# Optimization experiments

Hardware: AMD Instinct MI355X
Metric: run time of the kernel (lower is better)

The kernel has to match this reference:

```python
import jax, jax.numpy as jnp
import numpy as np

N, IN_DIM, HID, HEADS, HOPS, NCLS, E = 20000, 1536, 256, 4, 3, 3, 320000
HD = HID // HEADS
EPS = 1e-5
NEG_SLOPE = 0.2


def layer_norm(x, g, b):
    mu = jnp.mean(x, axis=-1, keepdims=True)
    var = jnp.var(x, axis=-1, keepdims=True)
    return (x - mu) * jax.lax.rsqrt(var + EPS) * g + b


def gatv2(x, src, dst, Wl, bl, Wr, br, att, bias):
    # x: [N, HID]; src/dst: [E'] (self loops included)
    xl = (x @ Wl + bl).reshape(N, HEADS, HD)  # source transform
    xr = (x @ Wr + br).reshape(N, HEADS, HD)  # target transform
    e = jax.nn.leaky_relu(xl[src] + xr[dst], NEG_SLOPE)          # [E', H, D]
    logits = jnp.einsum('ehd,hd->eh', e, att)                     # [E', H]
    m = jax.ops.segment_max(logits, dst, num_segments=N)         # [N, H]
    ex = jnp.exp(logits - m[dst])
    denom = jax.ops.segment_sum(ex, dst, num_segments=N)
    alpha = ex / denom[dst]                                       # softmax per dst
    msg = xl[src] * alpha[:, :, None]                             # [E', H, D]
    out = jax.ops.segment_sum(msg, dst, num_segments=N)
    return out.reshape(N, HID) + bias


def setup_inputs() -> dict:
    key = jax.random.key(0)
    ks = jax.random.split(key, 20)
    s = lambda k, shp, sc: jax.random.normal(k, shp, jnp.float32) * sc
    return {
        'features': s(ks[0], (N, IN_DIM), 1.0),
        'edge_index': jax.random.randint(ks[1], (2, E), 0, N, jnp.int64),
        'proj_W': s(ks[2], (IN_DIM, HID), 0.02),
        'proj_b': jnp.zeros((HID,), jnp.float32),
        'n0_g': jnp.ones((HID,), jnp.float32),
        'n0_b': jnp.zeros((HID,), jnp.float32),
        'Wl': s(ks[3], (HOPS, HID, HID), 0.05),
        'bl': jnp.zeros((HOPS, HID), jnp.float32),
        'Wr': s(ks[4], (HOPS, HID, HID), 0.05),
        'br': jnp.zeros((HOPS, HID), jnp.float32),
        'att': s(ks[5], (HOPS, HEADS, HD), 0.1),
        'gbias': jnp.zeros((HOPS, HID), jnp.float32),
        'ln_g': jnp.ones((HOPS, HID), jnp.float32),
        'ln_b': jnp.zeros((HOPS, HID), jnp.float32),
        'h1_W': s(ks[6], (HID, HID), 0.05),
        'h1_b': jnp.zeros((HID,), jnp.float32),
        'h2_W': s(ks[7], (HID, NCLS), 0.05),
        'h2_b': jnp.zeros((NCLS,), jnp.float32),
    }


def reference(features, edge_index, proj_W, proj_b, n0_g, n0_b, Wl, bl, Wr, br,
              att, gbias, ln_g, ln_b, h1_W, h1_b, h2_W, h2_b):
    # add self loops (PyG GATv2Conv default)
    loop = jnp.arange(N, dtype=edge_index.dtype)
    src = jnp.concatenate([edge_index[0], loop])
    dst = jnp.concatenate([edge_index[1], loop])

    x = layer_norm(features @ proj_W + proj_b, n0_g, n0_b)
    for h in range(HOPS):
        g = gatv2(x, src, dst, Wl[h], bl[h], Wr[h], br[h], att[h], gbias[h])
        x = layer_norm(g + x, ln_g[h], ln_b[h])
    # head (dropout inactive at eval); torch GELU is exact erf form
    x = jax.nn.gelu(x @ h1_W + h1_b, approximate=False)
    return x @ h2_W + h2_b
```

## Files before the change

kernel.cpp:

```cpp
#include <hip/hip_runtime.h>
#include <hip/hip_bf16.h>
#include <math.h>

#define NN 20000
#define INDIM 1536
#define HID 256
#define NE 320000
#define NEDGE (NE + NN)
#define EPSV 1e-5f
#define NEG 0.2f

typedef unsigned short ushort_b;
typedef unsigned int uint32;
typedef __bf16 bf16x8 __attribute__((ext_vector_type(8)));
typedef float f32x4 __attribute__((ext_vector_type(4)));

#define AS1(p) ((const __attribute__((address_space(1))) void*)(p))
#define AS3(p) ((__attribute__((address_space(3))) void*)(p))

__device__ inline ushort_b f2bf(float x) {
  union { float f; uint32 u; } v; v.f = x;
  uint32 r = v.u + 0x7FFFu + ((v.u >> 16) & 1u);
  return (ushort_b)(r >> 16);
}
__device__ inline float bf2f(ushort_b h) {
  union { uint32 u; float f; } v; v.u = ((uint32)h) << 16;
  return v.f;
}
__device__ inline float u2f(uint32 u) {
  union { uint32 u; float f; } v; v.u = u; return v.f;
}
__device__ inline uint32 cvtpk_bf16(float a, float b) {
  uint32 r;
  asm("v_cvt_pk_bf16_f32 %0, %1, %2" : "=v"(r) : "v"(a), "v"(b));
  return r;
}
__device__ inline float4 ldbf4(const ushort_b* p) {
  ushort4 u = *(const ushort4*)p;
  float4 f;
  f.x = bf2f(u.x); f.y = bf2f(u.y); f.z = bf2f(u.z); f.w = bf2f(u.w);
  return f;
}
__device__ inline float4 us4f(ushort4 u) {
  float4 f;
  f.x = bf2f(u.x); f.y = bf2f(u.y); f.z = bf2f(u.z); f.w = bf2f(u.w);
  return f;
}

template<int OUTMODE, int DUALB>
__global__ __launch_bounds__(256, 3) void gemm_mfma(
    const float* __restrict__ Af,
    const ushort_b* __restrict__ Bt0, const ushort_b* __restrict__ Bt1,
    const float* __restrict__ bias0, const float* __restrict__ bias1,
    void* __restrict__ C0, void* __restrict__ C1,
    int Mstore, int Kloop, int Kstride)
{
  __shared__ ushort_b Bs[3 * 8192];
  const ushort_b* Bt;
  const float* bias;
  void* Cv;
  int kbase;
  if (DUALB) {
    Bt = blockIdx.z ? Bt1 : Bt0;
    bias = blockIdx.z ? bias1 : bias0;
    Cv = blockIdx.z ? C1 : C0;
    kbase = 0;
  } else {
    Bt = Bt0;
    bias = blockIdx.z ? bias1 : bias0;
    Cv = (float*)C0 + (size_t)blockIdx.z * NN * HID;
    kbase = blockIdx.z * Kloop;
  }

  int tid = threadIdx.x;
  int wave = tid >> 6, lane = tid & 63;
  int quad = lane >> 4, mrow = lane & 15;
  int r0 = blockIdx.y * 128;
  int p  = blockIdx.x;
  int nk = Kloop >> 5;
  int nchunk = Kstride >> 5;
  int cb = kbase >> 5;

  int arow0 = r0 + (wave << 5) + mrow;
  int arow1 = arow0 + 16;
  if (arow0 >= Mstore) arow0 = Mstore - 1;
  if (arow1 >= Mstore) arow1 = Mstore - 1;
  const float* Aptr0 = Af + (size_t)arow0 * Kstride + kbase + (quad << 3);
  const float* Aptr1 = Af + (size_t)arow1 * Kstride + kbase + (quad << 3);

  f32x4 acc[2][8] = {};
  float pA0[16], pA1[16];

  auto issueB = [&](int kc, int buf) {
    const char* g = (const char*)Bt + (((size_t)(p * nchunk + (cb + kc))) << 14);
    char* l = (char*)Bs + buf * 16384;
    int o = tid << 4;
#pragma unroll
    for (int pl = 0; pl < 2; pl++) {
      int off = (pl << 13) + o;
      __builtin_amdgcn_global_load_lds(AS1(g + off), AS3(l + off), 16, 0, 0);
      __builtin_amdgcn_global_load_lds(AS1(g + off + 4096), AS3(l + off + 4096), 16, 0, 0);
    }
  };
  auto loadA = [&](int k, float* dst) {
    const float* s0 = Aptr0 + (k << 5);
    const float* s1 = Aptr1 + (k << 5);
    *(float4*)(dst)      = *(const float4*)(s0);
    *(float4*)(dst + 4)  = *(const float4*)(s0 + 4);
    *(float4*)(dst + 8)  = *(const float4*)(s1);
    *(float4*)(dst + 12) = *(const float4*)(s1 + 4);
  };
  auto cvtFrag = [&](const float* s, bf16x8& hh, bf16x8& ll) {
    union { bf16x8 v; uint32 u[4]; } H, L;
#pragma unroll
    for (int q2 = 0; q2 < 4; q2++) {
      float a = s[2 * q2], b = s[2 * q2 + 1];
      uint32 hp = cvtpk_bf16(a, b);
      float fa = u2f(hp << 16);
      float fb = u2f(hp & 0xffff0000u);
      H.u[q2] = hp;
      L.u[q2] = cvtpk_bf16(a - fa, b - fb);
    }
    hh = H.v; ll = L.v;
  };
  auto computeStage = [&](int buf, const bf16x8& ah0, const bf16x8& al0,
                          const bf16x8& ah1, const bf16x8& al1) {
    const ushort_b* bp = Bs + buf * 8192;
#pragma unroll
    for (int u = 0; u < 8; u++) {
      bf16x8 bh = *(const bf16x8*)(bp + (u << 9) + (lane << 3));
      bf16x8 bl = *(const bf16x8*)(bp + 4096 + (u << 9) + (lane << 3));
      acc[0][u] = __builtin_amdgcn_mfma_f32_16x16x32_bf16(ah0, bh, acc[0][u], 0, 0, 0);
      acc[0][u] = __builtin_amdgcn_mfma_f32_16x16x32_bf16(al0, bh, acc[0][u], 0, 0, 0);
      acc[0][u] = __builtin_amdgcn_mfma_f32_16x16x32_bf16(ah0, bl, acc[0][u], 0, 0, 0);
      acc[1][u] = __builtin_amdgcn_mfma_f32_16x16x32_bf16(ah1, bh, acc[1][u], 0, 0, 0);
      acc[1][u] = __builtin_amdgcn_mfma_f32_16x16x32_bf16(al1, bh, acc[1][u], 0, 0, 0);
      acc[1][u] = __builtin_amdgcn_mfma_f32_16x16x32_bf16(ah1, bl, acc[1][u], 0, 0, 0);
    }
  };

  loadA(0, pA0);
  issueB(0, 0);
  issueB(1, 1);
  loadA(1, pA1);
  asm volatile("s_waitcnt vmcnt(8)" ::: "memory");
  __builtin_amdgcn_sched_barrier(0);
  __builtin_amdgcn_s_barrier();
  __builtin_amdgcn_sched_barrier(0);

  int bcur = 0;
  for (int k = 0; k < nk; k += 2) {
    int b1 = bcur + 1; if (b1 >= 3) b1 -= 3;
    int b2 = bcur + 2; if (b2 >= 3) b2 -= 3;

    {
      bf16x8 ah0, al0, ah1, al1;
      cvtFrag(pA0, ah0, al0);
      cvtFrag(pA0 + 8, ah1, al1);
      if (k + 2 < nk) { issueB(k + 2, b2); loadA(k + 2, pA0); }
      computeStage(bcur, ah0, al0, ah1, al1);
      if (k + 2 < nk) { asm volatile("s_waitcnt vmcnt(8)" ::: "memory"); }
      else            { asm volatile("s_waitcnt vmcnt(4)" ::: "memory"); }
      __builtin_amdgcn_sched_barrier(0);
      __builtin_amdgcn_s_barrier();
      __builtin_amdgcn_sched_barrier(0);
    }
    {
      bf16x8 ah0, al0, ah1, al1;
      cvtFrag(pA1, ah0, al0);
      cvtFrag(pA1 + 8, ah1, al1);
      if (k + 3 < nk) { issueB(k + 3, bcur); loadA(k + 3, pA1); }
      computeStage(b1, ah0, al0, ah1, al1);
      if (k + 3 < nk) {
        asm volatile("s_waitcnt vmcnt(8)" ::: "memory");
        __builtin_amdgcn_sched_barrier(0);
        __builtin_amdgcn_s_barrier();
        __builtin_amdgcn_sched_barrier(0);
      }
    }
    bcur = b2;
  }

#pragma unroll
  for (int u = 0; u < 8; u++) {
    int col = (p << 7) + (u << 4) + mrow;
    float bb = bias[col];
#pragma unroll
    for (int t = 0; t < 2; t++) {
#pragma unroll
      for (int r = 0; r < 4; r++) {
        int row = r0 + (wave << 5) + (t << 4) + (quad << 2) + r;
        if (row < Mstore) {
          float v = acc[t][u][r] + bb;
          if (OUTMODE == 3) v = 0.5f * v * (1.f + erff(v * 0.70710678118654752f));
          if (OUTMODE == 2) ((ushort_b*)Cv)[(size_t)row * 256 + col] = f2bf(v);
          else              ((float*)Cv)[(size_t)row * 256 + col] = v;
        }
      }
    }
  }
}

__device__ inline void prep_body(const float* __restrict__ W, int ldw, int nchunk,
                                 ushort_b* __restrict__ out, int c, int p, int tid)
{
  ushort_b* base = out + (((size_t)(p * nchunk + c)) << 13);
#pragma unroll
  for (int g0 = 0; g0 < 2; g0++) {
    int g = tid + (g0 << 8);
    int u = g >> 6, l = g & 63;
    int quad = l >> 4, mrow = l & 15;
    int col = (p << 7) + (u << 4) + mrow;
    int krow = (c << 5) + (quad << 3);
    uint32 hu[4], lu[4];
#pragma unroll
    for (int q2 = 0; q2 < 4; q2++) {
      float a = W[(size_t)(krow + 2 * q2) * ldw + col];
      float b = W[(size_t)(krow + 2 * q2 + 1) * ldw + col];
      ushort_b h0 = f2bf(a), h1 = f2bf(b);
      hu[q2] = (uint32)h0 | ((uint32)h1 << 16);
      lu[q2] = (uint32)f2bf(a - bf2f(h0)) | ((uint32)f2bf(b - bf2f(h1)) << 16);
    }
    *(uint4*)(base + (size_t)g * 8)        = make_uint4(hu[0], hu[1], hu[2], hu[3]);
    *(uint4*)(base + 4096 + (size_t)g * 8) = make_uint4(lu[0], lu[1], lu[2], lu[3]);
  }
}

__global__ __launch_bounds__(256) void prep_frag(
    const float* __restrict__ W, int ldw, int nchunk, ushort_b* __restrict__ out)
{
  prep_body(W, ldw, nchunk, out, blockIdx.x, blockIdx.y, threadIdx.x);
}

__global__ __launch_bounds__(256) void prep_frag7(
    const float* __restrict__ Wl, const float* __restrict__ Wr,
    const float* __restrict__ h1W, ushort_b* __restrict__ dst)
{
  int z = blockIdx.z;
  const float* W = (z < 3) ? Wl + (size_t)z * 65536
                 : (z < 6) ? Wr + (size_t)(z - 3) * 65536
                           : h1W;
  prep_body(W, 256, 8, dst + (size_t)z * 131072, blockIdx.x, blockIdx.y, threadIdx.x);
}

__global__ __launch_bounds__(256) void ln_sum_kernel(
    const float* __restrict__ in,
    const float* __restrict__ g, const float* __restrict__ b,
    float* __restrict__ out, int n)
{
  int wave = threadIdx.x >> 6, lane = threadIdx.x & 63;
  int row = blockIdx.x * 4 + wave;
  if (row >= n) return;
  int c = lane << 2;
  const float* p0 = in + (size_t)row * HID + c;
  float4 v  = *(const float4*)(p0);
  float4 v1 = *(const float4*)(p0 + (size_t)NN * HID);
  float4 v2 = *(const float4*)(p0 + (size_t)2 * NN * HID);
  float4 v3 = *(const float4*)(p0 + (size_t)3 * NN * HID);
  v.x += v1.x + v2.x + v3.x;
  v.y += v1.y + v2.y + v3.y;
  v.z += v1.z + v2.z + v3.z;
  v.w += v1.w + v2.w + v3.w;
  float s1 = v.x + v.y + v.z + v.w;
  float s2 = v.x * v.x + v.y * v.y + v.z * v.z + v.w * v.w;
#pragma unroll
  for (int m = 1; m < 64; m <<= 1) {
    s1 += __shfl_xor(s1, m, 64);
    s2 += __shfl_xor(s2, m, 64);
  }
  float mu = s1 * (1.f / 256.f);
  float var = s2 * (1.f / 256.f) - mu * mu;
  float rstd = rsqrtf(var + EPSV);
  float4 gv = *(const float4*)(g + c);
  float4 bv = *(const float4*)(b + c);
  float4 o;
  o.x = (v.x - mu) * rstd * gv.x + bv.x;
  o.y = (v.y - mu) * rstd * gv.y + bv.y;
  o.z = (v.z - mu) * rstd * gv.z + bv.z;
  o.w = (v.w - mu) * rstd * gv.w + bv.w;
  *(float4*)(out + (size_t)row * HID + c) = o;
}

__global__ void count_kernel(const int* __restrict__ ei, int* __restrict__ cnt)
{
  int e = blockIdx.x * blockDim.x + threadIdx.x;
  if (e < NEDGE) {
    int d = (e < NE) ? ei[NE + e] : (e - NE);
    atomicAdd(&cnt[d], 1);
  }
}

__global__ __launch_bounds__(1024) void scan_kernel(
    const int* __restrict__ cnt, int* __restrict__ offs, int* __restrict__ cursor)
{
  __shared__ int sums[1024];
  int tid = threadIdx.x;
  const int CH = 20;
  int base = tid * CH;
  int loc[CH];
  int s = 0;
#pragma unroll
  for (int i = 0; i < CH; i++) {
    int idx = base + i;
    int v = (idx < NN) ? cnt[idx] : 0;
    loc[i] = s;
    s += v;
  }
  sums[tid] = s;
  __syncthreads();
  for (int off = 1; off < 1024; off <<= 1) {
    int t = (tid >= off) ? sums[tid - off] : 0;
    __syncthreads();
    sums[tid] += t;
    __syncthreads();
  }
  int pre = (tid == 0) ? 0 : sums[tid - 1];
#pragma unroll
  for (int i = 0; i < CH; i++) {
    int idx = base + i;
    if (idx < NN) { int e = pre + loc[i]; offs[idx] = e; cursor[idx] = e; }
  }
  if (tid == 0) offs[NN] = NEDGE;
}

__global__ void scatter_kernel(const int* __restrict__ ei, int* __restrict__ cursor,
                               int* __restrict__ csr_src)
{
  int e = blockIdx.x * blockDim.x + threadIdx.x;
  if (e < NEDGE) {
    int s, d;
    if (e < NE) { s = ei[e]; d = ei[NE + e]; }
    else { s = e - NE; d = e - NE; }
    int p = atomicAdd(&cursor[d], 1);
    csr_src[p] = s;
  }
}

__device__ inline float edge_logit(float4 xv, float4 xrv, float4 attv) {
  float e0 = xv.x + xrv.x, e1 = xv.y + xrv.y, e2 = xv.z + xrv.z, e3 = xv.w + xrv.w;
  e0 = (e0 > 0.f) ? e0 : NEG * e0;
  e1 = (e1 > 0.f) ? e1 : NEG * e1;
  e2 = (e2 > 0.f) ? e2 : NEG * e2;
  e3 = (e3 > 0.f) ? e3 : NEG * e3;
  float lc = e0 * attv.x + e1 * attv.y + e2 * attv.z + e3 * attv.w;
  lc += __shfl_xor(lc, 1, 16);
  lc += __shfl_xor(lc, 2, 16);
  lc += __shfl_xor(lc, 4, 16);
  lc += __shfl_xor(lc, 8, 16);
  return lc;
}

#define ACCUM(i, wt, xv) {                             \
    lS[i] += wt;                                       \
    pS##i##0 += wt * xv.x; pS##i##1 += wt * xv.y;      \
    pS##i##2 += wt * xv.z; pS##i##3 += wt * xv.w; }

__global__ __launch_bounds__(256) void gat_kernel(
    const ushort_b* __restrict__ xl, const ushort_b* __restrict__ xr,
    const float* __restrict__ x_in, const float* __restrict__ att,
    const float* __restrict__ gbias, const float* __restrict__ ln_g,
    const float* __restrict__ ln_b, const int* __restrict__ offs,
    const int* __restrict__ csr_src, float* __restrict__ x_out)
{
  int wave = threadIdx.x >> 6, lane = threadIdx.x & 63;
  int node = blockIdx.x * 4 + wave;
  int c = lane << 2;
  float4 xrv = ldbf4(xr + (size_t)node * HID + c);
  float4 attv = *(const float4*)(att + c);

  float lS[4] = {0.f, 0.f, 0.f, 0.f};
  float pS00 = 0.f, pS01 = 0.f, pS02 = 0.f, pS03 = 0.f;
  float pS10 = 0.f, pS11 = 0.f, pS12 = 0.f, pS13 = 0.f;
  float pS20 = 0.f, pS21 = 0.f, pS22 = 0.f, pS23 = 0.f;
  float pS30 = 0.f, pS31 = 0.f, pS32 = 0.f, pS33 = 0.f;

  int e = offs[node], end = offs[node + 1];
  int last = end - 1;

  int s1i = e + 1 <= last ? e + 1 : last;
  int s2i = e + 2 <= last ? e + 2 : last;
  int s3i = e + 3 <= last ? e + 3 : last;
  int i0 = csr_src[e], i1 = csr_src[s1i], i2 = csr_src[s2i], i3 = csr_src[s3i];
  ushort4 a0 = *(const ushort4*)(xl + (size_t)i0 * HID + c);
  ushort4 a1 = *(const ushort4*)(xl + (size_t)i1 * HID + c);
  ushort4 a2 = *(const ushort4*)(xl + (size_t)i2 * HID + c);
  ushort4 a3 = *(const ushort4*)(xl + (size_t)i3 * HID + c);

  for (;;) {
    int rem = end - e;
    int en = e + 4;
    bool more = en < end;
    ushort4 b0, b1, b2, b3;
    if (more) {
      int t1i = en + 1 <= last ? en + 1 : last;
      int t2i = en + 2 <= last ? en + 2 : last;
      int t3i = en + 3 <= last ? en + 3 : last;
      int j0 = csr_src[en], j1 = csr_src[t1i], j2 = csr_src[t2i], j3 = csr_src[t3i];
      b0 = *(const ushort4*)(xl + (size_t)j0 * HID + c);
      b1 = *(const ushort4*)(xl + (size_t)j1 * HID + c);
      b2 = *(const ushort4*)(xl + (size_t)j2 * HID + c);
      b3 = *(const ushort4*)(xl + (size_t)j3 * HID + c);
    }
    float4 x0v = us4f(a0);
    float4 x1v = us4f(a1);
    float4 x2v = us4f(a2);
    float4 x3v = us4f(a3);
    float g0 = edge_logit(x0v, xrv, attv);
    float g1 = edge_logit(x1v, xrv, attv);
    float g2 = edge_logit(x2v, xrv, attv);
    float g3 = edge_logit(x3v, xrv, attv);
    float w0 = __expf(g0);
    float w1 = (rem > 1) ? __expf(g1) : 0.f;
    float w2 = (rem > 2) ? __expf(g2) : 0.f;
    float w3 = (rem > 3) ? __expf(g3) : 0.f;
    ACCUM(0, w0, x0v);
    ACCUM(1, w1, x1v);
    ACCUM(2, w2, x2v);
    ACCUM(3, w3, x3v);
    if (!more) break;
    e = en;
    a0 = b0; a1 = b1; a2 = b2; a3 = b3;
  }

  float l  = lS[0] + lS[1] + lS[2] + lS[3];
  float q0 = pS00 + pS10 + pS20 + pS30;
  float q1 = pS01 + pS11 + pS21 + pS31;
  float q2 = pS02 + pS12 + pS22 + pS32;
  float q3 = pS03 + pS13 + pS23 + pS33;

  float inv = 1.f / l;
  float4 xv = *(const float4*)(x_in + (size_t)node * HID + c);
  float4 gb = *(const float4*)(gbias + c);
  float o0 = q0 * inv + gb.x + xv.x;
  float o1 = q1 * inv + gb.y + xv.y;
  float o2 = q2 * inv + gb.z + xv.z;
  float o3 = q3 * inv + gb.w + xv.w;
  float s1s = o0 + o1 + o2 + o3;
  float s2s = o0 * o0 + o1 * o1 + o2 * o2 + o3 * o3;
#pragma unroll
  for (int mmk = 1; mmk < 64; mmk <<= 1) {
    s1s += __shfl_xor(s1s, mmk, 64);
    s2s += __shfl_xor(s2s, mmk, 64);
  }
  float mu = s1s * (1.f / 256.f);
  float var = s2s * (1.f / 256.f) - mu * mu;
  float rstd = rsqrtf(var + EPSV);
  float4 gv = *(const float4*)(ln_g + c);
  float4 bv = *(const float4*)(ln_b + c);
  float4 o;
  o.x = (o0 - mu) * rstd * gv.x + bv.x;
  o.y = (o1 - mu) * rstd * gv.y + bv.y;
  o.z = (o2 - mu) * rstd * gv.z + bv.z;
  o.w = (o3 - mu) * rstd * gv.w + bv.w;
  *(float4*)(x_out + (size_t)node * HID + c) = o;
}

__global__ __launch_bounds__(256) void head2_kernel(
    const float* __restrict__ t1, const float* __restrict__ W,
    const float* __restrict__ bias, float* __restrict__ out)
{
  int wave = threadIdx.x >> 6, lane = threadIdx.x & 63;
  int row = blockIdx.x * 4 + wave;
  if (row >= NN) return;
  int c = lane << 2;
  float4 v = *(const float4*)(t1 + (size_t)row * HID + c);
  float p0 = 0.f, p1 = 0.f, p2 = 0.f;
#pragma unroll
  for (int j = 0; j < 4; j++) {
    float vj = (&v.x)[j];
    p0 += vj * W[(c + j) * 3 + 0];
    p1 += vj * W[(c + j) * 3 + 1];
    p2 += vj * W[(c + j) * 3 + 2];
  }
#pragma unroll
  for (int mm = 1; mm < 64; mm <<= 1) {
    p0 += __shfl_xor(p0, mm, 64);
    p1 += __shfl_xor(p1, mm, 64);
    p2 += __shfl_xor(p2, mm, 64);
  }
  if (lane == 0) {
    out[(size_t)row * 3 + 0] = p0 + bias[0];
    out[(size_t)row * 3 + 1] = p1 + bias[1];
    out[(size_t)row * 3 + 2] = p2 + bias[2];
  }
}

extern "C" void kernel_launch(void* const* d_in, const int* in_sizes, int n_in,
                              void* d_out, int out_size, void* d_ws, size_t ws_size,
                              hipStream_t stream)
{
  const float* features = (const float*)d_in[0];
  const int*   ei       = (const int*)d_in[1];
  const float* proj_W   = (const float*)d_in[2];
  const float* proj_b   = (const float*)d_in[3];
  const float* n0_g     = (const float*)d_in[4];
  const float* n0_b     = (const float*)d_in[5];
  const float* Wl       = (const float*)d_in[6];
  const float* bl       = (const float*)d_in[7];
  const float* Wr       = (const float*)d_in[8];
  const float* br       = (const float*)d_in[9];
  const float* att      = (const float*)d_in[10];
  const float* gbias    = (const float*)d_in[11];
  const float* ln_g     = (const float*)d_in[12];
  const float* ln_b     = (const float*)d_in[13];
  const float* h1_W     = (const float*)d_in[14];
  const float* h1_b     = (const float*)d_in[15];
  const float* h2_W     = (const float*)d_in[16];
  const float* h2_b     = (const float*)d_in[17];
  float* out = (float*)d_out;

  char* w = (char*)d_ws;
  float*    x0    = (float*)w;    w += (size_t)NN * HID * 4;
  float*    x1    = (float*)w;    w += (size_t)NN * HID * 4;
  float*    part1 = (float*)w;    w += (size_t)NN * HID * 4;
  ushort_b* xlb   = (ushort_b*)w; w += (size_t)NN * HID * 2;
  ushort_b* xrb   = (ushort_b*)w; w += (size_t)NN * HID * 2;
  ushort_b* wtp   = (ushort_b*)w; w += (size_t)2 * HID * INDIM * 2;
  ushort_b* w7    = (ushort_b*)w; w += (size_t)14 * HID * HID * 2;
  float* zbias = (float*)w; w += (size_t)HID * 4;
  int* cnt     = (int*)w;  w += (size_t)NN * 4;
  int* offs    = (int*)w;  w += (size_t)(NN + 1) * 4;
  int* cursor  = (int*)w;  w += (size_t)NN * 4;
  int* csr     = (int*)w;  w += (size_t)NEDGE * 4;

  hipMemsetAsync(cnt, 0, (size_t)NN * 4, stream);
  hipMemsetAsync(zbias, 0, (size_t)HID * 4, stream);
  count_kernel<<<(NEDGE + 255) / 256, 256, 0, stream>>>(ei, cnt);
  scan_kernel<<<1, 1024, 0, stream>>>(cnt, offs, cursor);
  scatter_kernel<<<(NEDGE + 255) / 256, 256, 0, stream>>>(ei, cursor, csr);

  prep_frag<<<dim3(INDIM / 32, 2), 256, 0, stream>>>(proj_W, HID, INDIM / 32, wtp);
  prep_frag7<<<dim3(8, 2, 7), 256, 0, stream>>>(Wl, Wr, h1_W, w7);

  const int MB = (NN + 127) / 128;
  dim3 gproj(2, MB, 4);
  dim3 ghop(2, MB, 2);
  dim3 gsingle(2, MB, 1);

  gemm_mfma<0, 0><<<gproj, 256, 0, stream>>>(
      features, wtp, wtp, proj_b, zbias, x0, x0, NN, INDIM / 4, INDIM);
  ln_sum_kernel<<<(NN + 3) / 4, 256, 0, stream>>>(x0, n0_g, n0_b, x0, NN);

  float* xcur = x0;
  float* xnxt = x1;
  for (int h = 0; h < 3; h++) {
    gemm_mfma<2, 1><<<ghop, 256, 0, stream>>>(
        xcur, w7 + (size_t)h * 131072, w7 + (size_t)(3 + h) * 131072,
        bl + h * HID, br + h * HID, xlb, xrb, NN, HID, HID);
    gat_kernel<<<NN / 4, 256, 0, stream>>>(
        xlb, xrb, xcur, att + h * HID, gbias + h * HID,
        ln_g + h * HID, ln_b + h * HID, offs, csr, xnxt);
    float* t = xcur; xcur = xnxt; xnxt = t;
  }

  gemm_mfma<3, 1><<<gsingle, 256, 0, stream>>>(
      xcur, w7 + (size_t)6 * 131072, w7 + (size_t)6 * 131072,
      h1_b, h1_b, part1, part1, NN, HID, HID);
  head2_kernel<<<(NN + 3) / 4, 256, 0, stream>>>(part1, h2_W, h2_b, out);
}
```

Baseline: 603.7 us.

## Merge prep kernels, halve projection split-K, deepen GAT index prefetch

Merges the two weight-fragment prep kernels into one launch and folds the zbias memset into count_kernel, which cuts launch count. Changes the projection GEMM split-K from 4 to 2 slices, so the LN reduction kernel reads two partials instead of four. The GAT kernel now loads CSR source indices two batches ahead and adds a launch-bounds occupancy hint. Fewer K-slices means fewer GEMM blocks and less parallelism, but less partial-sum traffic.

```diff
diff --git a/kernel.cpp b/kernel.cpp
--- a/kernel.cpp
+++ b/kernel.cpp
@@ -226,21 +226,21 @@
   }
 }
 
-__global__ __launch_bounds__(256) void prep_frag(
-    const float* __restrict__ W, int ldw, int nchunk, ushort_b* __restrict__ out)
-{
-  prep_body(W, ldw, nchunk, out, blockIdx.x, blockIdx.y, threadIdx.x);
-}
-
-__global__ __launch_bounds__(256) void prep_frag7(
-    const float* __restrict__ Wl, const float* __restrict__ Wr,
-    const float* __restrict__ h1W, ushort_b* __restrict__ dst)
-{
-  int z = blockIdx.z;
-  const float* W = (z < 3) ? Wl + (size_t)z * 65536
-                 : (z < 6) ? Wr + (size_t)(z - 3) * 65536
-                           : h1W;
-  prep_body(W, 256, 8, dst + (size_t)z * 131072, blockIdx.x, blockIdx.y, threadIdx.x);
+__global__ __launch_bounds__(256) void prep_all(
+    const float* __restrict__ projW, const float* __restrict__ Wl,
+    const float* __restrict__ Wr, const float* __restrict__ h1W,
+    ushort_b* __restrict__ wtp, ushort_b* __restrict__ w7)
+{
+  int z = blockIdx.z, c = blockIdx.x, p = blockIdx.y;
+  if (z == 7) {
+    prep_body(projW, HID, INDIM / 32, wtp, c, p, threadIdx.x);
+  } else {
+    if (c >= 8) return;
+    const float* W = (z < 3) ? Wl + (size_t)z * 65536
+                   : (z < 6) ? Wr + (size_t)(z - 3) * 65536
+                             : h1W;
+    prep_body(W, 256, 8, w7 + (size_t)z * 131072, c, p, threadIdx.x);
+  }
 }
 
 __global__ __launch_bounds__(256) void ln_sum_kernel(
@@ -255,12 +255,7 @@
   const float* p0 = in + (size_t)row * HID + c;
   float4 v  = *(const float4*)(p0);
   float4 v1 = *(const float4*)(p0 + (size_t)NN * HID);
-  float4 v2 = *(const float4*)(p0 + (size_t)2 * NN * HID);
-  float4 v3 = *(const float4*)(p0 + (size_t)3 * NN * HID);
-  v.x += v1.x + v2.x + v3.x;
-  v.y += v1.y + v2.y + v3.y;
-  v.z += v1.z + v2.z + v3.z;
-  v.w += v1.w + v2.w + v3.w;
+  v.x += v1.x; v.y += v1.y; v.z += v1.z; v.w += v1.w;
   float s1 = v.x + v.y + v.z + v.w;
   float s2 = v.x * v.x + v.y * v.y + v.z * v.z + v.w * v.w;
 #pragma unroll
@@ -281,9 +276,11 @@
   *(float4*)(out + (size_t)row * HID + c) = o;
 }
 
-__global__ void count_kernel(const int* __restrict__ ei, int* __restrict__ cnt)
+__global__ void count_kernel(const int* __restrict__ ei, int* __restrict__ cnt,
+                             float* __restrict__ zbias)
 {
   int e = blockIdx.x * blockDim.x + threadIdx.x;
+  if (e < HID) zbias[e] = 0.f;
   if (e < NEDGE) {
     int d = (e < NE) ? ei[NE + e] : (e - NE);
     atomicAdd(&cnt[d], 1);
@@ -355,7 +352,7 @@
     pS##i##0 += wt * xv.x; pS##i##1 += wt * xv.y;      \
     pS##i##2 += wt * xv.z; pS##i##3 += wt * xv.w; }
 
-__global__ __launch_bounds__(256) void gat_kernel(
+__global__ __launch_bounds__(256, 6) void gat_kernel(
     const ushort_b* __restrict__ xl, const ushort_b* __restrict__ xr,
     const float* __restrict__ x_in, const float* __restrict__ att,
     const float* __restrict__ gbias, const float* __restrict__ ln_g,
@@ -376,30 +373,31 @@
 
   int e = offs[node], end = offs[node + 1];
   int last = end - 1;
-
-  int s1i = e + 1 <= last ? e + 1 : last;
-  int s2i = e + 2 <= last ? e + 2 : last;
-  int s3i = e + 3 <= last ? e + 3 : last;
-  int i0 = csr_src[e], i1 = csr_src[s1i], i2 = csr_src[s2i], i3 = csr_src[s3i];
-  ushort4 a0 = *(const ushort4*)(xl + (size_t)i0 * HID + c);
-  ushort4 a1 = *(const ushort4*)(xl + (size_t)i1 * HID + c);
-  ushort4 a2 = *(const ushort4*)(xl + (size_t)i2 * HID + c);
-  ushort4 a3 = *(const ushort4*)(xl + (size_t)i3 * HID + c);
+#define CI(x) ((x) <= last ? (x) : last)
+  auto G = [&](int i) { return *(const ushort4*)(xl + (size_t)i * HID + c); };
+
+  int i0 = csr_src[e], i1 = csr_src[CI(e + 1)];
+  int i2 = csr_src[CI(e + 2)], i3 = csr_src[CI(e + 3)];
+  ushort4 a0 = G(i0), a1 = G(i1), a2 = G(i2), a3 = G(i3);
+  int en = e + 4;
+  bool more = en < end;
+  int j0, j1, j2, j3;
+  if (more) {
+    j0 = csr_src[en]; j1 = csr_src[CI(en + 1)];
+    j2 = csr_src[CI(en + 2)]; j3 = csr_src[CI(en + 3)];
+  }
 
   for (;;) {
     int rem = end - e;
-    int en = e + 4;
-    bool more = en < end;
+    int en2 = en + 4;
+    bool more2 = more && (en2 < end);
     ushort4 b0, b1, b2, b3;
     if (more) {
-      int t1i = en + 1 <= last ? en + 1 : last;
-      int t2i = en + 2 <= last ? en + 2 : last;
-      int t3i = en + 3 <= last ? en + 3 : last;
-      int j0 = csr_src[en], j1 = csr_src[t1i], j2 = csr_src[t2i], j3 = csr_src[t3i];
-      b0 = *(const ushort4*)(xl + (size_t)j0 * HID + c);
-      b1 = *(const ushort4*)(xl + (size_t)j1 * HID + c);
-      b2 = *(const ushort4*)(xl + (size_t)j2 * HID + c);
-      b3 = *(const ushort4*)(xl + (size_t)j3 * HID + c);
+      b0 = G(j0); b1 = G(j1); b2 = G(j2); b3 = G(j3);
+      if (more2) {
+        j0 = csr_src[en2]; j1 = csr_src[CI(en2 + 1)];
+        j2 = csr_src[CI(en2 + 2)]; j3 = csr_src[CI(en2 + 3)];
+      }
     }
     float4 x0v = us4f(a0);
     float4 x1v = us4f(a1);
@@ -418,9 +416,10 @@
     ACCUM(2, w2, x2v);
     ACCUM(3, w3, x3v);
     if (!more) break;
-    e = en;
+    e = en; en = en2; more = more2;
     a0 = b0; a1 = b1; a2 = b2; a3 = b3;
   }
+#undef CI
 
   float l  = lS[0] + lS[1] + lS[2] + lS[3];
   float q0 = pS00 + pS10 + pS20 + pS30;
@@ -524,21 +523,18 @@
   int* csr     = (int*)w;  w += (size_t)NEDGE * 4;
 
   hipMemsetAsync(cnt, 0, (size_t)NN * 4, stream);
-  hipMemsetAsync(zbias, 0, (size_t)HID * 4, stream);
-  count_kernel<<<(NEDGE + 255) / 256, 256, 0, stream>>>(ei, cnt);
+  count_kernel<<<(NEDGE + 255) / 256, 256, 0, stream>>>(ei, cnt, zbias);
   scan_kernel<<<1, 1024, 0, stream>>>(cnt, offs, cursor);
   scatter_kernel<<<(NEDGE + 255) / 256, 256, 0, stream>>>(ei, cursor, csr);
-
-  prep_frag<<<dim3(INDIM / 32, 2), 256, 0, stream>>>(proj_W, HID, INDIM / 32, wtp);
-  prep_frag7<<<dim3(8, 2, 7), 256, 0, stream>>>(Wl, Wr, h1_W, w7);
+  prep_all<<<dim3(INDIM / 32, 2, 8), 256, 0, stream>>>(proj_W, Wl, Wr, h1_W, wtp, w7);
 
   const int MB = (NN + 127) / 128;
-  dim3 gproj(2, MB, 4);
+  dim3 gproj(2, MB, 2);
   dim3 ghop(2, MB, 2);
   dim3 gsingle(2, MB, 1);
 
   gemm_mfma<0, 0><<<gproj, 256, 0, stream>>>(
-      features, wtp, wtp, proj_b, zbias, x0, x0, NN, INDIM / 4, INDIM);
+      features, wtp, wtp, proj_b, zbias, x0, x0, NN, INDIM / 2, INDIM);
   ln_sum_kernel<<<(NN + 3) / 4, 256, 0, stream>>>(x0, n0_g, n0_b, x0, NN);
 
   float* xcur = x0;
```

Measured after the change: 578.8 us. 1.04x faster.
